# Kernel optimization log

Hardware: AMD Instinct MI355X
Metric: run time of the kernel (lower is better)

Reference implementation:

```python
import jax, jax.numpy as jnp
import numpy as np

BS, H, W, C = 32, 64, 64, 256
SEQ = 32


def setup_inputs() -> dict:
    key = jax.random.key(0)
    k1, k2, k3, k4, k5 = jax.random.split(key, 5)
    x = jax.random.normal(k1, (BS, H, W, C), dtype=jnp.float32)
    sentence = jax.random.normal(k2, (BS, C), dtype=jnp.float32)  # unused in call()
    context = jax.random.normal(k3, (BS, SEQ, C), dtype=jnp.float32)
    mask = jax.random.bernoulli(k4, 0.3, (BS, SEQ))
    W_word = jax.random.normal(k5, (C, C), dtype=jnp.float32) * (1.0 / np.sqrt(C))
    return {"x": x, "sentence": sentence, "context": context, "mask": mask, "W_word": W_word}


def reference(x, sentence, context, mask, W_word):
    bs, h, w, c = x.shape
    hw = h * w
    seq = context.shape[1]
    xf = x.reshape(bs, hw, c)                                   # [bs, hw, C]
    ctx = jnp.einsum('bsd,dc->bsc', context, W_word)            # conv1x1 word projection
    attn = jnp.einsum('bnc,bsc->bns', xf, ctx)                  # [bs, hw, seq]
    attn = attn.reshape(bs * hw, seq)
    # faithful to original: mask tiled hw times along axis 0 (block-repeat order)
    mask_t = jnp.tile(mask, (hw, 1))                            # [bs*hw, seq]
    neg_inf = jnp.asarray(-jnp.inf, dtype=attn.dtype)
    attn = jnp.where(mask_t, neg_inf, attn)
    attn = jax.nn.softmax(attn, axis=-1).reshape(bs, hw, seq)
    # matmul(ctx^T, attn^T) -> [bs, C, hw] -> transpose -> [bs, hw, C]
    weighted_context = jnp.einsum('bsc,bns->bnc', ctx, attn).reshape(bs, h, w, c)
    word_attn = attn.reshape(bs, h, w, seq)
    return weighted_context, word_attn
```

## Files before the change

### kernel.cpp

```cpp
#include <hip/hip_runtime.h>
#include <stdint.h>

typedef __attribute__((ext_vector_type(8))) short short8;
typedef __attribute__((ext_vector_type(4))) float float4v;

#define HW   4096
#define CC   256
#define SEQQ 32
#define BSZ  32
#define ROWS 64
#define PSTR 48

static __device__ __forceinline__ uint16_t f2bf(float f) {
  union { float f; uint32_t u; } v; v.f = f;
  uint32_t r = v.u + 0x7FFFu + ((v.u >> 16) & 1u);
  return (uint16_t)(r >> 16);
}
static __device__ __forceinline__ float bf2f(uint16_t h) {
  union { uint32_t u; float f; } v; v.u = ((uint32_t)h) << 16;
  return v.f;
}

extern "C" __global__ __launch_bounds__(256) void prep_kernel(
    const float* __restrict__ ctx_in,
    const float* __restrict__ Wp,
    const void*  __restrict__ mask,
    float* __restrict__ bias_ws,
    uint16_t* __restrict__ ctx_hi_ws,
    uint16_t* __restrict__ ctx_lo_ws,
    uint16_t* __restrict__ ctxT_ws)
{
  const int t = threadIdx.x;
  if (blockIdx.x == 256) {
    __shared__ int byteFlag;
    if (t == 0) byteFlag = 0;
    __syncthreads();
    const uint8_t* mb = (const uint8_t*)mask;
    int nz = 0;
    for (int i = t; i < 1024; i += 256)
      if ((i & 3) == 1 && mb[i] != 0) nz = 1;
    if (nz) atomicOr(&byteFlag, 1);
    __syncthreads();
    const bool byteMode = (byteFlag != 0);
    const uint32_t* mw = (const uint32_t*)mask;
    for (int i = t; i < 1024; i += 256) {
      bool m = byteMode ? (mb[i] != 0) : (mw[i] != 0);
      bias_ws[i] = m ? -1e30f : 0.0f;
    }
    return;
  }

  const int r0 = blockIdx.x * 4;
  __shared__ float crow[4][CC];
  #pragma unroll
  for (int j = 0; j < 4; ++j)
    crow[j][t] = ctx_in[(size_t)(r0 + j) * CC + t];
  __syncthreads();

  float acc[4] = {0.f, 0.f, 0.f, 0.f};
  for (int d = 0; d < CC; ++d) {
    float wv = Wp[(size_t)d * CC + t];
    #pragma unroll
    for (int j = 0; j < 4; ++j) acc[j] += crow[j][d] * wv;
  }
  #pragma unroll
  for (int j = 0; j < 4; ++j) {
    int row = r0 + j;
    int bb = row >> 5, ss = row & 31;
    float v = acc[j];
    uint16_t h = f2bf(v);
    uint16_t lo = f2bf(v - bf2f(h));
    ctx_hi_ws[(size_t)row * CC + t] = h;
    ctx_lo_ws[(size_t)row * CC + t] = lo;
    ctxT_ws[((size_t)bb * CC + t) * SEQQ + ss] = h;
  }
}

extern "C" __global__ __launch_bounds__(256) void attn_main(
    const float* __restrict__ x,
    const uint8_t* __restrict__ ws,
    float* __restrict__ out0,
    float* __restrict__ out1)
{
  const float*    bias_ws   = (const float*)ws;
  const uint16_t* ctx_hi_ws = (const uint16_t*)(ws + 4096);
  const uint16_t* ctx_lo_ws = ctx_hi_ws + BSZ * SEQQ * CC;
  const uint16_t* ctxT_ws   = ctx_lo_ws + BSZ * SEQQ * CC;

  __shared__ __align__(16) uint16_t ctxHi[SEQQ * 264];
  __shared__ __align__(16) uint16_t ctxLo[SEQQ * 264];
  __shared__ __align__(16) uint16_t ctxT[CC * PSTR];
  __shared__ __align__(16) float    biasL[BSZ * SEQQ];
  __shared__ __align__(16) uint16_t pL[ROWS * PSTR];

  const int tid = threadIdx.x;
  const int b   = blockIdx.y;
  const int n0  = blockIdx.x * ROWS;

  {
    const uint4* s_hi = (const uint4*)(ctx_hi_ws + (size_t)b * SEQQ * CC);
    const uint4* s_lo = (const uint4*)(ctx_lo_ws + (size_t)b * SEQQ * CC);
    const uint4* s_T  = (const uint4*)(ctxT_ws  + (size_t)b * CC * SEQQ);
    for (int i = tid; i < 1024; i += 256) {
      int row = i >> 5, col = i & 31;
      *(uint4*)&ctxHi[row * 264 + col * 8] = s_hi[i];
      *(uint4*)&ctxLo[row * 264 + col * 8] = s_lo[i];
    }
    for (int i = tid; i < 1024; i += 256) {
      int c = i >> 2, col = i & 3;
      *(uint4*)&ctxT[c * PSTR + col * 8] = s_T[i];
    }
    ((uint4*)biasL)[tid] = ((const uint4*)bias_ws)[tid];
  }
  __syncthreads();

  const int w    = tid >> 6;
  const int lane = tid & 63;
  const int l15  = lane & 15;
  const int quad = lane >> 4;
  const int nbase = n0 + w * 16;

  float4v acc0 = {0.f, 0.f, 0.f, 0.f};
  float4v acc1 = {0.f, 0.f, 0.f, 0.f};
  const float* xrow = x + ((size_t)b * HW + nbase + l15) * CC + quad * 8;

  for (int k0 = 0; k0 < 8; ++k0) {
    float4 xa = *(const float4*)(xrow + k0 * 32);
    float4 xb = *(const float4*)(xrow + k0 * 32 + 4);
    float xv[8] = {xa.x, xa.y, xa.z, xa.w, xb.x, xb.y, xb.z, xb.w};
    short8 ah, al;
    #pragma unroll
    for (int j = 0; j < 8; ++j) {
      uint16_t h = f2bf(xv[j]);
      ah[j] = (short)h;
      al[j] = (short)f2bf(xv[j] - bf2f(h));
    }
    const int kb = k0 * 32 + quad * 8;
    short8 bh0 = *(const short8*)&ctxHi[l15 * 264 + kb];
    short8 bl0 = *(const short8*)&ctxLo[l15 * 264 + kb];
    short8 bh1 = *(const short8*)&ctxHi[(16 + l15) * 264 + kb];
    short8 bl1 = *(const short8*)&ctxLo[(16 + l15) * 264 + kb];
    acc0 = __builtin_amdgcn_mfma_f32_16x16x32_bf16(ah, bh0, acc0, 0, 0, 0);
    acc0 = __builtin_amdgcn_mfma_f32_16x16x32_bf16(ah, bl0, acc0, 0, 0, 0);
    acc0 = __builtin_amdgcn_mfma_f32_16x16x32_bf16(al, bh0, acc0, 0, 0, 0);
    acc1 = __builtin_amdgcn_mfma_f32_16x16x32_bf16(ah, bh1, acc1, 0, 0, 0);
    acc1 = __builtin_amdgcn_mfma_f32_16x16x32_bf16(ah, bl1, acc1, 0, 0, 0);
    acc1 = __builtin_amdgcn_mfma_f32_16x16x32_bf16(al, bh1, acc1, 0, 0, 0);
  }

  #pragma unroll
  for (int r = 0; r < 4; ++r) {
    const int n  = nbase + quad * 4 + r;
    const int br = n & 31;
    float v0 = acc0[r] + biasL[br * 32 + l15];
    float v1 = acc1[r] + biasL[br * 32 + 16 + l15];
    float mx = fmaxf(v0, v1);
    #pragma unroll
    for (int off = 1; off < 16; off <<= 1)
      mx = fmaxf(mx, __shfl_xor(mx, off, 64));
    float e0 = __expf(v0 - mx);
    float e1 = __expf(v1 - mx);
    float sm = e0 + e1;
    #pragma unroll
    for (int off = 1; off < 16; off <<= 1)
      sm += __shfl_xor(sm, off, 64);
    float inv = 1.0f / sm;
    float p0 = e0 * inv, p1 = e1 * inv;
    size_t o1 = ((size_t)b * HW + n) * SEQQ;
    out1[o1 + l15]      = p0;
    out1[o1 + 16 + l15] = p1;
    pL[(w * 16 + quad * 4 + r) * PSTR + l15]      = f2bf(p0);
    pL[(w * 16 + quad * 4 + r) * PSTR + 16 + l15] = f2bf(p1);
  }
  __syncthreads();

  short8 pa = *(const short8*)&pL[(w * 16 + l15) * PSTR + quad * 8];
  #pragma unroll
  for (int ct = 0; ct < 16; ++ct) {
    short8 bfr = *(const short8*)&ctxT[(ct * 16 + l15) * PSTR + quad * 8];
    float4v z = {0.f, 0.f, 0.f, 0.f};
    float4v d = __builtin_amdgcn_mfma_f32_16x16x32_bf16(pa, bfr, z, 0, 0, 0);
    #pragma unroll
    for (int r = 0; r < 4; ++r) {
      size_t o0 = ((size_t)b * HW + nbase + quad * 4 + r) * CC + ct * 16 + l15;
      out0[o0] = d[r];
    }
  }
}

extern "C" void kernel_launch(void* const* d_in, const int* in_sizes, int n_in,
                              void* d_out, int out_size, void* d_ws, size_t ws_size,
                              hipStream_t stream) {
  const float* x      = (const float*)d_in[0];
  const float* ctx_in = (const float*)d_in[2];
  const void*  mask   = d_in[3];
  const float* Wp     = (const float*)d_in[4];

  float* out0 = (float*)d_out;
  float* out1 = out0 + (size_t)BSZ * HW * CC;

  uint8_t*  ws        = (uint8_t*)d_ws;
  float*    bias_ws   = (float*)ws;
  uint16_t* ctx_hi_ws = (uint16_t*)(ws + 4096);
  uint16_t* ctx_lo_ws = ctx_hi_ws + BSZ * SEQQ * CC;
  uint16_t* ctxT_ws   = ctx_lo_ws + BSZ * SEQQ * CC;

  prep_kernel<<<257, 256, 0, stream>>>(ctx_in, Wp, mask, bias_ws,
                                       ctx_hi_ws, ctx_lo_ws, ctxT_ws);
  attn_main<<<dim3(HW / ROWS, BSZ), 256, 0, stream>>>(x, ws, out0, out1);
}
```

Baseline: 284.1 us.

## Share one swizzled ctx layout across both GEMMs and bit-pack the mask

```diff
diff --git a/kernel.cpp b/kernel.cpp
--- a/kernel.cpp
+++ b/kernel.cpp
@@ -9,7 +9,10 @@
 #define SEQQ 32
 #define BSZ  32
 #define ROWS 64
-#define PSTR 48
+
+#define SGRP     1032
+#define CTXT_SZ  (8 * SGRP)
+#define PSTR_P   40
 
 static __device__ __forceinline__ uint16_t f2bf(float f) {
   union { float f; uint32_t u; } v; v.f = f;
@@ -25,10 +28,9 @@
     const float* __restrict__ ctx_in,
     const float* __restrict__ Wp,
     const void*  __restrict__ mask,
-    float* __restrict__ bias_ws,
-    uint16_t* __restrict__ ctx_hi_ws,
-    uint16_t* __restrict__ ctx_lo_ws,
-    uint16_t* __restrict__ ctxT_ws)
+    uint32_t* __restrict__ maskbits_ws,
+    uint16_t* __restrict__ hiT_ws,
+    uint16_t* __restrict__ loT_ws)
 {
   const int t = threadIdx.x;
   if (blockIdx.x == 256) {
@@ -42,75 +44,80 @@
     if (nz) atomicOr(&byteFlag, 1);
     __syncthreads();
     const bool byteMode = (byteFlag != 0);
-    const uint32_t* mw = (const uint32_t*)mask;
-    for (int i = t; i < 1024; i += 256) {
-      bool m = byteMode ? (mb[i] != 0) : (mw[i] != 0);
-      bias_ws[i] = m ? -1e30f : 0.0f;
+    const uint32_t* mw32 = (const uint32_t*)mask;
+    if (t < 32) {
+      uint32_t bits = 0;
+      for (int s = 0; s < 32; ++s) {
+        bool m = byteMode ? (mb[t * 32 + s] != 0) : (mw32[t * 32 + s] != 0);
+        if (m) bits |= (1u << s);
+      }
+      maskbits_ws[t] = bits;
     }
     return;
   }
 
   const int r0 = blockIdx.x * 4;
   __shared__ float crow[4][CC];
+  for (int i = t; i < 1024; i += 256)
+    crow[i >> 8][i & 255] = ctx_in[(size_t)r0 * CC + i];
+  __syncthreads();
+
+  const int j  = t >> 6;
+  const int c4 = (t & 63) << 2;
+  float4v acc = {0.f, 0.f, 0.f, 0.f};
+  #pragma unroll 8
+  for (int d = 0; d < CC; ++d) {
+    float s = crow[j][d];
+    const float4 wv = *(const float4*)&Wp[(size_t)d * CC + c4];
+    acc[0] += s * wv.x; acc[1] += s * wv.y;
+    acc[2] += s * wv.z; acc[3] += s * wv.w;
+  }
+
+  const int row = r0 + j, bb = row >> 5, ss = row & 31;
+  const size_t base = (size_t)bb * CTXT_SZ + (ss >> 2) * SGRP + (ss & 3) * 16;
   #pragma unroll
-  for (int j = 0; j < 4; ++j)
-    crow[j][t] = ctx_in[(size_t)(r0 + j) * CC + t];
-  __syncthreads();
-
-  float acc[4] = {0.f, 0.f, 0.f, 0.f};
-  for (int d = 0; d < CC; ++d) {
-    float wv = Wp[(size_t)d * CC + t];
-    #pragma unroll
-    for (int j = 0; j < 4; ++j) acc[j] += crow[j][d] * wv;
-  }
-  #pragma unroll
-  for (int j = 0; j < 4; ++j) {
-    int row = r0 + j;
-    int bb = row >> 5, ss = row & 31;
-    float v = acc[j];
-    uint16_t h = f2bf(v);
-    uint16_t lo = f2bf(v - bf2f(h));
-    ctx_hi_ws[(size_t)row * CC + t] = h;
-    ctx_lo_ws[(size_t)row * CC + t] = lo;
-    ctxT_ws[((size_t)bb * CC + t) * SEQQ + ss] = h;
-  }
-}
-
-extern "C" __global__ __launch_bounds__(256) void attn_main(
+  for (int q = 0; q < 4; ++q) {
+    const int c = c4 + q;
+    const float v = acc[q];
+    const uint16_t h  = f2bf(v);
+    const uint16_t lo = f2bf(v - bf2f(h));
+    const size_t idx = base + (c >> 4) * 64 + (c & 15);
+    hiT_ws[idx] = h;
+    loT_ws[idx] = lo;
+  }
+}
+
+extern "C" __global__ __launch_bounds__(256, 4) void attn_main(
     const float* __restrict__ x,
     const uint8_t* __restrict__ ws,
     float* __restrict__ out0,
     float* __restrict__ out1)
 {
-  const float*    bias_ws   = (const float*)ws;
-  const uint16_t* ctx_hi_ws = (const uint16_t*)(ws + 4096);
-  const uint16_t* ctx_lo_ws = ctx_hi_ws + BSZ * SEQQ * CC;
-  const uint16_t* ctxT_ws   = ctx_lo_ws + BSZ * SEQQ * CC;
-
-  __shared__ __align__(16) uint16_t ctxHi[SEQQ * 264];
-  __shared__ __align__(16) uint16_t ctxLo[SEQQ * 264];
-  __shared__ __align__(16) uint16_t ctxT[CC * PSTR];
-  __shared__ __align__(16) float    biasL[BSZ * SEQQ];
-  __shared__ __align__(16) uint16_t pL[ROWS * PSTR];
+  const uint32_t* maskbits_ws = (const uint32_t*)ws;
+  const uint16_t* hiT_ws = (const uint16_t*)(ws + 128);
+  const uint16_t* loT_ws = hiT_ws + (size_t)BSZ * CTXT_SZ;
+
+  __shared__ __align__(16) uint16_t hiT[CTXT_SZ];
+  __shared__ __align__(16) uint16_t loT[CTXT_SZ];
+  __shared__ __align__(16) uint16_t pL[ROWS * PSTR_P];
+  __shared__ uint32_t maskW[32];
 
   const int tid = threadIdx.x;
   const int b   = blockIdx.y;
   const int n0  = blockIdx.x * ROWS;
 
   {
-    const uint4* s_hi = (const uint4*)(ctx_hi_ws + (size_t)b * SEQQ * CC);
-    const uint4* s_lo = (const uint4*)(ctx_lo_ws + (size_t)b * SEQQ * CC);
-    const uint4* s_T  = (const uint4*)(ctxT_ws  + (size_t)b * CC * SEQQ);
-    for (int i = tid; i < 1024; i += 256) {
-      int row = i >> 5, col = i & 31;
-      *(uint4*)&ctxHi[row * 264 + col * 8] = s_hi[i];
-      *(uint4*)&ctxLo[row * 264 + col * 8] = s_lo[i];
-    }
-    for (int i = tid; i < 1024; i += 256) {
-      int c = i >> 2, col = i & 3;
-      *(uint4*)&ctxT[c * PSTR + col * 8] = s_T[i];
-    }
-    ((uint4*)biasL)[tid] = ((const uint4*)bias_ws)[tid];
+    const uint4* sHi = (const uint4*)(hiT_ws + (size_t)b * CTXT_SZ);
+    const uint4* sLo = (const uint4*)(loT_ws + (size_t)b * CTXT_SZ);
+    uint4* dHi = (uint4*)hiT;
+    uint4* dLo = (uint4*)loT;
+    #pragma unroll
+    for (int k = 0; k < 4; ++k) {
+      dHi[tid + k * 256] = sHi[tid + k * 256];
+      dLo[tid + k * 256] = sLo[tid + k * 256];
+    }
+    if (tid < 8) { dHi[1024 + tid] = sHi[1024 + tid]; dLo[1024 + tid] = sLo[1024 + tid]; }
+    if (tid < 32) maskW[tid] = maskbits_ws[tid];
   }
   __syncthreads();
 
@@ -123,6 +130,7 @@
   float4v acc0 = {0.f, 0.f, 0.f, 0.f};
   float4v acc1 = {0.f, 0.f, 0.f, 0.f};
   const float* xrow = x + ((size_t)b * HW + nbase + l15) * CC + quad * 8;
+  const int sbase = (l15 >> 2) * SGRP + (l15 & 3) * 16 + (quad >> 1) * 64 + (quad & 1) * 8;
 
   for (int k0 = 0; k0 < 8; ++k0) {
     float4 xa = *(const float4*)(xrow + k0 * 32);
@@ -130,16 +138,17 @@
     float xv[8] = {xa.x, xa.y, xa.z, xa.w, xb.x, xb.y, xb.z, xb.w};
     short8 ah, al;
     #pragma unroll
-    for (int j = 0; j < 8; ++j) {
-      uint16_t h = f2bf(xv[j]);
-      ah[j] = (short)h;
-      al[j] = (short)f2bf(xv[j] - bf2f(h));
-    }
-    const int kb = k0 * 32 + quad * 8;
-    short8 bh0 = *(const short8*)&ctxHi[l15 * 264 + kb];
-    short8 bl0 = *(const short8*)&ctxLo[l15 * 264 + kb];
-    short8 bh1 = *(const short8*)&ctxHi[(16 + l15) * 264 + kb];
-    short8 bl1 = *(const short8*)&ctxLo[(16 + l15) * 264 + kb];
+    for (int jj = 0; jj < 8; ++jj) {
+      uint32_t u = __float_as_uint(xv[jj]);
+      ah[jj] = (short)(u >> 16);
+      float r = xv[jj] - __uint_as_float(u & 0xFFFF0000u);
+      al[jj] = (short)(__float_as_uint(r) >> 16);
+    }
+    const int ka = sbase + k0 * 128;
+    short8 bh0 = *(const short8*)&hiT[ka];
+    short8 bl0 = *(const short8*)&loT[ka];
+    short8 bh1 = *(const short8*)&hiT[ka + 4 * SGRP];
+    short8 bl1 = *(const short8*)&loT[ka + 4 * SGRP];
     acc0 = __builtin_amdgcn_mfma_f32_16x16x32_bf16(ah, bh0, acc0, 0, 0, 0);
     acc0 = __builtin_amdgcn_mfma_f32_16x16x32_bf16(ah, bl0, acc0, 0, 0, 0);
     acc0 = __builtin_amdgcn_mfma_f32_16x16x32_bf16(al, bh0, acc0, 0, 0, 0);
@@ -150,10 +159,10 @@
 
   #pragma unroll
   for (int r = 0; r < 4; ++r) {
-    const int n  = nbase + quad * 4 + r;
-    const int br = n & 31;
-    float v0 = acc0[r] + biasL[br * 32 + l15];
-    float v1 = acc1[r] + biasL[br * 32 + 16 + l15];
+    const int n = nbase + quad * 4 + r;
+    const uint32_t mwd = maskW[n & 31];
+    float v0 = (mwd & (1u << l15))        ? -1e30f : acc0[r];
+    float v1 = (mwd & (1u << (l15 + 16))) ? -1e30f : acc1[r];
     float mx = fmaxf(v0, v1);
     #pragma unroll
     for (int off = 1; off < 16; off <<= 1)
@@ -169,15 +178,18 @@
     size_t o1 = ((size_t)b * HW + n) * SEQQ;
     out1[o1 + l15]      = p0;
     out1[o1 + 16 + l15] = p1;
-    pL[(w * 16 + quad * 4 + r) * PSTR + l15]      = f2bf(p0);
-    pL[(w * 16 + quad * 4 + r) * PSTR + 16 + l15] = f2bf(p1);
-  }
-  __syncthreads();
-
-  short8 pa = *(const short8*)&pL[(w * 16 + l15) * PSTR + quad * 8];
+    pL[(w * 16 + quad * 4 + r) * PSTR_P + l15]      = f2bf(p0);
+    pL[(w * 16 + quad * 4 + r) * PSTR_P + 16 + l15] = f2bf(p1);
+  }
+
+  short8 pa = *(const short8*)&pL[(w * 16 + l15) * PSTR_P + quad * 8];
+  const int cbase = quad * 2 * SGRP + l15;
   #pragma unroll
   for (int ct = 0; ct < 16; ++ct) {
-    short8 bfr = *(const short8*)&ctxT[(ct * 16 + l15) * PSTR + quad * 8];
+    short8 bfr;
+    #pragma unroll
+    for (int jj = 0; jj < 8; ++jj)
+      bfr[jj] = (short)hiT[cbase + (jj >> 2) * SGRP + ct * 64 + (jj & 3) * 16];
     float4v z = {0.f, 0.f, 0.f, 0.f};
     float4v d = __builtin_amdgcn_mfma_f32_16x16x32_bf16(pa, bfr, z, 0, 0, 0);
     #pragma unroll
@@ -199,13 +211,12 @@
   float* out0 = (float*)d_out;
   float* out1 = out0 + (size_t)BSZ * HW * CC;
 
-  uint8_t*  ws        = (uint8_t*)d_ws;
-  float*    bias_ws   = (float*)ws;
-  uint16_t* ctx_hi_ws = (uint16_t*)(ws + 4096);
-  uint16_t* ctx_lo_ws = ctx_hi_ws + BSZ * SEQQ * CC;
-  uint16_t* ctxT_ws   = ctx_lo_ws + BSZ * SEQQ * CC;
-
-  prep_kernel<<<257, 256, 0, stream>>>(ctx_in, Wp, mask, bias_ws,
-                                       ctx_hi_ws, ctx_lo_ws, ctxT_ws);
+  uint8_t*  ws          = (uint8_t*)d_ws;
+  uint32_t* maskbits_ws = (uint32_t*)ws;
+  uint16_t* hiT_ws      = (uint16_t*)(ws + 128);
+  uint16_t* loT_ws      = hiT_ws + (size_t)BSZ * CTXT_SZ;
+
+  prep_kernel<<<257, 256, 0, stream>>>(ctx_in, Wp, mask, maskbits_ws,
+                                       hiT_ws, loT_ws);
   attn_main<<<dim3(HW / ROWS, BSZ), 256, 0, stream>>>(x, ws, out0, out1);
 }
```

Result: no change. 289.7 us (+2.0%).
